# Performance work log

Hardware: AMD Instinct MI355X
Metric: run time of the kernel (lower is better)

## Reference

```python
import jax, jax.numpy as jnp
import numpy as np

B, S, D, H, I, E, K, L, C = 4, 1024, 512, 8, 2048, 8, 2, 4, 4
D2 = D // 2
EPS = 1e-5  # torch LayerNorm default


def _ln(x, w, b):
    m = jnp.mean(x, -1, keepdims=True)
    v = jnp.mean((x - m) ** 2, -1, keepdims=True)
    return (x - m) * jax.lax.rsqrt(v + EPS) * w + b


def setup_inputs() -> dict:
    key = jax.random.key(0)
    ks = iter(jax.random.split(key, 40))
    n = lambda shp, s=0.02: jax.random.normal(next(ks), shp, dtype=jnp.float32) * s
    return {
        'embeddings': jax.random.normal(next(ks), (B, S, D), jnp.float32),
        'attention_mask': jnp.ones((B, S), jnp.float32),
        'in_w': n((L, 3 * D, D)), 'in_b': jnp.zeros((L, 3 * D)),
        'out_w': n((L, D, D)), 'out_b': jnp.zeros((L, D)),
        'ln1_w': jnp.ones((L, D)), 'ln1_b': jnp.zeros((L, D)),
        'ln2_w': jnp.ones((L, D)), 'ln2_b': jnp.zeros((L, D)),
        'gate_w': n((L, E, D)),
        'e_w1': n((L, E, D, I)), 'e_b1': jnp.zeros((L, E, I)),
        'e_w2': n((L, E, I, D)), 'e_b2': jnp.zeros((L, E, D)),
        'mln_w': jnp.ones((L, D)), 'mln_b': jnp.zeros((L, D)),
        'fln_w': jnp.ones((D,)), 'fln_b': jnp.zeros((D,)),
        'pool_w': n((D, D)), 'pool_b': jnp.zeros((D,)),
        'cls_w': n((C, D)), 'cls_b': jnp.zeros((C,)),
        'cf_w1': n((D2, D)), 'cf_b1': jnp.zeros((D2,)),
        'cf_w2': n((1, D2)), 'cf_b2': jnp.zeros((1,)),
    }


def _forward(embeddings, attention_mask, in_w, in_b, out_w, out_b, ln1_w, ln1_b,
             ln2_w, ln2_b, gate_w, e_w1, e_b1, e_w2, e_b2, mln_w, mln_b,
             fln_w, fln_b, pool_w, pool_b, cls_w, cls_b, cf_w1, cf_b1, cf_w2, cf_b2):
    x = embeddings
    dh = D // H
    total_aux = jnp.float32(0.0)
    for l in range(L):
        # --- self-attention (eval mode, dropout off) ---
        h = _ln(x, ln1_w[l], ln1_b[l])
        qkv = h @ in_w[l].T + in_b[l]                       # (B,S,3D)
        q, k, v = jnp.split(qkv, 3, axis=-1)
        q = q.reshape(B, S, H, dh).transpose(0, 2, 1, 3)
        k = k.reshape(B, S, H, dh).transpose(0, 2, 1, 3)
        v = v.reshape(B, S, H, dh).transpose(0, 2, 1, 3)
        scores = jnp.einsum('bhqd,bhkd->bhqk', q, k) / (dh ** 0.5)
        attn = jax.nn.softmax(scores, axis=-1)
        ctx = jnp.einsum('bhqk,bhkd->bhqd', attn, v).transpose(0, 2, 1, 3).reshape(B, S, D)
        x = x + (ctx @ out_w[l].T + out_b[l])
        # --- MoE FFN (residual is the post-norm2 tensor, per source) ---
        h = _ln(x, ln2_w[l], ln2_b[l])
        flat = h.reshape(-1, D)                             # (T,D)
        probs = jax.nn.softmax(flat @ gate_w[l].T, axis=-1) # (T,E)
        vals, idx = jax.lax.top_k(probs, K)                 # (T,K)
        vals = vals / vals.sum(-1, keepdims=True)
        onehot = jax.nn.one_hot(idx, E, dtype=flat.dtype)   # (T,K,E)
        comb = jnp.einsum('tk,tke->te', vals, onehot)       # (T,E) per-expert weight, 0 if not selected
        mid = jax.nn.gelu(jnp.einsum('td,edf->tef', flat, e_w1[l]) + e_b1[l], approximate=False)
        eout = jnp.einsum('tef,efd->ted', mid, e_w2[l]) + e_b2[l]
        moe_out = jnp.einsum('ted,te->td', eout, comb).reshape(B, S, D)
        moe_out = moe_out * attention_mask[..., None]
        x = _ln(h + moe_out, mln_w[l], mln_b[l])
        usage = onehot.sum((0, 1)) / flat.shape[0]
        total_aux = total_aux + jnp.mean((usage - 1.0 / E) ** 2)
    # --- head ---
    x = _ln(x, fln_w, fln_b)
    me = attention_mask[..., None]
    pooled = (x * me).sum(1) / jnp.maximum(me.sum(1), 1e-9)
    pooled = jnp.tanh(pooled @ pool_w.T + pool_b)
    logits = pooled @ cls_w.T + cls_b
    conf = jax.nn.sigmoid(jax.nn.relu(pooled @ cf_w1.T + cf_b1) @ cf_w2.T + cf_b2)
    return logits, total_aux / L, conf


def reference(embeddings, attention_mask, in_w, in_b, out_w, out_b, ln1_w, ln1_b,
              ln2_w, ln2_b, gate_w, e_w1, e_b1, e_w2, e_b2, mln_w, mln_b,
              fln_w, fln_b, pool_w, pool_b, cls_w, cls_b, cf_w1, cf_b1, cf_w2, cf_b2):
    return _forward(embeddings, attention_mask, in_w, in_b, out_w, out_b, ln1_w, ln1_b,
                    ln2_w, ln2_b, gate_w, e_w1, e_b1, e_w2, e_b2, mln_w, mln_b,
                    fln_w, fln_b, pool_w, pool_b, cls_w, cls_b, cf_w1, cf_b1, cf_w2, cf_b2)
```

## Files before the change

kernel.cpp:

```cpp
#include <hip/hip_runtime.h>
#include <math.h>

#define B_ 4
#define S_ 1024
#define D_ 512
#define H_ 8
#define DH_ 64
#define I_ 2048
#define E_ 8
#define L_ 4
#define T_ 4096

using bf16x8 = __attribute__((ext_vector_type(8))) __bf16;
using f32x4  = __attribute__((ext_vector_type(4))) float;

typedef __attribute__((address_space(1))) const void gvoid;
typedef __attribute__((address_space(3))) void lvoid;
__device__ __forceinline__ void gl_lds16(const void* g, void* l){
  __builtin_amdgcn_global_load_lds((gvoid*)g, (lvoid*)l, 16, 0, 0);
}

__device__ __forceinline__ float wred_sum(float v){
#pragma unroll
  for(int m=32;m>0;m>>=1) v += __shfl_xor(v, m, 64);
  return v;
}
__device__ __forceinline__ unsigned short f2bf(float f){
  unsigned x = __float_as_uint(f);
  unsigned r = (x + 0x7FFFu + ((x>>16)&1u)) >> 16;
  return (unsigned short)r;
}
__device__ __forceinline__ float bf2f(unsigned short u){
  return __uint_as_float(((unsigned)u)<<16);
}
__device__ __forceinline__ unsigned pk2(float a, float b){
  return (unsigned)f2bf(a) | ((unsigned)f2bf(b)<<16);
}

template<int BM, int BN, bool MOE, bool GATHER, bool OUT_BF16, int ACT, bool ADD_IN, bool VT>
__global__ __launch_bounds__(512)
void gemm_k(const unsigned short* __restrict__ A, const unsigned short* __restrict__ Bv,
            void* Cp, const float* __restrict__ bias, const float* addin,
            int M, int N, int K, int lda, int ldb, int ldc,
            int hdiv, long sAb, long sAh, long sBb, long sBh, long sCb, long sCh,
            float scale,
            const int* __restrict__ moff, const int* __restrict__ mcnt,
            const int* __restrict__ rowtok, const int* __restrict__ btab,
            long sBe, int biasStride, int nby, unsigned short* __restrict__ vtp)
{
  constexpr int BK = 64;
  constexpr int WM = BM/2, WN = BN/4, FM = WM/16, FNN = WN/16;
  constexpr int RPC = 64;
  constexpr int SHPC = 4096;
  constexpr int NA = BM/RPC, NB = BN/RPC;
  __shared__ unsigned short As[2*BM*BK];
  __shared__ unsigned short Bs[2*BN*BK];

  const int tid = threadIdx.x, wid = tid>>6, lane = tid&63;
  const int wy = wid>>2, wx = wid&3, ln16 = lane&15;

  const int nwg = gridDim.x, cpx = nwg >> 3;
  const int lin = blockIdx.x;
  const int wg  = (lin & 7)*cpx + (lin >> 3);
  const int bxi = wg / nby, byi = wg % nby;

  int m0 = bxi*BM;
  const int n0 = byi*BN;

  float* Cf = nullptr; unsigned short* Ch = nullptr;
  const float* biasp = bias;
  const unsigned short* Bp = Bv;
  int seg = 0, cnt = M;

  if constexpr (MOE){
    int tv = btab[bxi];
    if (tv < 0) return;
    int e = tv>>8;
    m0 = (tv&255)*BM;
    seg = moff[e]; cnt = mcnt[e];
    Bp = Bv + (long)e*sBe;
    if constexpr (OUT_BF16) Ch = (unsigned short*)Cp; else Cf = (float*)Cp;
    if (biasp) biasp += (long)e*biasStride;
  } else {
    int z = blockIdx.z, zb = z/hdiv, zh = z%hdiv;
    A  += (long)zb*sAb + (long)zh*sAh;
    Bp += (long)zb*sBb + (long)zh*sBh;
    long coff = (long)zb*sCb + (long)zh*sCh;
    if constexpr (OUT_BF16) Ch = (unsigned short*)Cp + coff; else Cf = ((float*)Cp) + coff;
    if constexpr (ADD_IN) addin += coff;
  }

  const int srow = tid >> 3;
  const int scol = ((tid & 7) ^ (srow & 7)) * 8;
  long ga[NA], gb[NB];
#pragma unroll
  for (int j=0; j<NA; j++){
    int r = m0 + j*RPC + srow;
    if constexpr (MOE){
      r = min(r, cnt-1);
      long gr = GATHER ? (long)rowtok[seg+r] : (long)(seg+r);
      ga[j] = gr*lda + scol;
    } else {
      ga[j] = (long)min(r, M-1)*lda + scol;
    }
  }
#pragma unroll
  for (int j=0; j<NB; j++){
    int bn = min(n0 + j*RPC + srow, N-1);
    gb[j] = (long)bn*ldb + scol;
  }

  f32x4 acc[FM][FNN];
#pragma unroll
  for(int i=0;i<FM;i++)
#pragma unroll
    for(int j=0;j<FNN;j++){ f32x4 z = {0.f,0.f,0.f,0.f}; acc[i][j] = z; }

  const int nt = K/BK;
  const int rsw = ln16 & 7;
  const int u0 = ((lane>>4)     ^ rsw) * 8;
  const int u1 = ((4+(lane>>4)) ^ rsw) * 8;

#pragma unroll
  for (int j=0; j<NA; j++) gl_lds16(A + ga[j], As + j*SHPC + wid*512);
#pragma unroll
  for (int j=0; j<NB; j++) gl_lds16(Bp + gb[j], Bs + j*SHPC + wid*512);

  for (int t = 0; t < nt; ++t){
    const int cb = t & 1;
    const unsigned short* Ab = As + cb*BM*BK;
    const unsigned short* Bb = Bs + cb*BN*BK;
    unsigned short* An = As + (cb^1)*BM*BK;
    unsigned short* Bn = Bs + (cb^1)*BN*BK;
    const bool pf = (t+1 < nt);
    const long k0n = (long)(t+1)*BK;

    asm volatile("s_waitcnt vmcnt(0)" ::: "memory");
    __builtin_amdgcn_s_barrier();
    __builtin_amdgcn_sched_barrier(0);

    if (pf){
#pragma unroll
      for (int j=0; j<NA; j++) gl_lds16(A + ga[j] + k0n, An + j*SHPC + wid*512);
    }
    {
      bf16x8 fa[FM], fb[FNN];
#pragma unroll
      for(int i=0;i<FM;i++) fa[i] = *(const bf16x8*)&Ab[(wy*WM + i*16 + ln16)*BK + u0];
#pragma unroll
      for(int j=0;j<FNN;j++) fb[j] = *(const bf16x8*)&Bb[(wx*WN + j*16 + ln16)*BK + u0];
      __builtin_amdgcn_s_setprio(1);
#pragma unroll
      for(int i=0;i<FM;i++)
#pragma unroll
        for(int j=0;j<FNN;j++)
          acc[i][j] = __builtin_amdgcn_mfma_f32_16x16x32_bf16(fa[i], fb[j], acc[i][j], 0, 0, 0);
      __builtin_amdgcn_s_setprio(0);
    }
    if (pf){
#pragma unroll
      for (int j=0; j<NB; j++) gl_lds16(Bp + gb[j] + k0n, Bn + j*SHPC + wid*512);
    }
    {
      bf16x8 fa[FM], fb[FNN];
#pragma unroll
      for(int i=0;i<FM;i++) fa[i] = *(const bf16x8*)&Ab[(wy*WM + i*16 + ln16)*BK + u1];
#pragma unroll
      for(int j=0;j<FNN;j++) fb[j] = *(const bf16x8*)&Bb[(wx*WN + j*16 + ln16)*BK + u1];
      __builtin_amdgcn_s_setprio(1);
#pragma unroll
      for(int i=0;i<FM;i++)
#pragma unroll
        for(int j=0;j<FNN;j++)
          acc[i][j] = __builtin_amdgcn_mfma_f32_16x16x32_bf16(fa[i], fb[j], acc[i][j], 0, 0, 0);
      __builtin_amdgcn_s_setprio(0);
    }
  }

  if constexpr (VT){
    if (n0 >= 1024){
#pragma unroll
      for(int i=0;i<FM;i++){
        int mbase = m0 + wy*WM + i*16 + (lane>>4)*4;
        int bb = mbase >> 10;
        int k4 = mbase & 1023;
#pragma unroll
        for(int j=0;j<FNN;j++){
          int n = n0 + wx*WN + j*16 + ln16;
          float bv = biasp ? biasp[n] : 0.f;
          int hh = (n - 1024) >> 6, dd = (n - 1024) & 63;
          f32x4 v = acc[i][j];
          ushort4 pkv;
          pkv.x = f2bf(v[0]*scale + bv);
          pkv.y = f2bf(v[1]*scale + bv);
          pkv.z = f2bf(v[2]*scale + bv);
          pkv.w = f2bf(v[3]*scale + bv);
          *(ushort4*)(vtp + (long)(bb*8 + hh)*65536 + (long)dd*1024 + k4) = pkv;
        }
      }
      return;
    }
  }

#pragma unroll
  for(int i=0;i<FM;i++){
    int mbase = m0 + wy*WM + i*16 + (lane>>4)*4;
#pragma unroll
    for(int j=0;j<FNN;j++){
      int n = n0 + wx*WN + j*16 + ln16;
      float bv = biasp ? biasp[n] : 0.f;
      f32x4 v = acc[i][j];
#pragma unroll
      for(int r=0;r<4;r++){
        int m = mbase + r;
        if (m < cnt){
          float x = v[r]*scale + bv;
          if constexpr (ACT == 1) x = 0.5f*x*(1.f + erff(x*0.70710678118654752f));
          long ci = (long)(MOE ? seg + m : m)*ldc + n;
          if constexpr (ADD_IN) x += addin[ci];
          if constexpr (OUT_BF16) Ch[ci] = f2bf(x);
          else Cf[ci] = x;
        }
      }
    }
  }
}

__global__ __launch_bounds__(256)
void flash_k(const unsigned short* __restrict__ qkvb, const unsigned short* __restrict__ Vt,
             unsigned short* __restrict__ ctx)
{
  __shared__ unsigned short Pl[4][16*72];
  const int qt = blockIdx.x, z = blockIdx.y, b = z>>3, h = z&7;
  const int wid = threadIdx.x>>6, lane = threadIdx.x&63;
  const int ln16 = lane&15, g = lane>>4;
  const int q0 = qt*64 + wid*16;
  unsigned short* Pw = &Pl[wid][0];

  const unsigned short* Qp = qkvb + (long)(b*1024 + q0 + ln16)*1536 + h*64 + g*8;
  bf16x8 qf0 = *(const bf16x8*)Qp;
  bf16x8 qf1 = *(const bf16x8*)(Qp + 32);
  const unsigned short* Kbase = qkvb + (long)b*1024*1536 + 512 + h*64 + g*8;
  const unsigned short* Vbase = Vt + (long)z*65536 + g*8;

  float m_s[4], l_s[4];
  f32x4 oacc[4];
#pragma unroll
  for(int r=0;r<4;r++){ m_s[r] = -1e30f; l_s[r] = 0.f; }
#pragma unroll
  for(int j=0;j<4;j++){ f32x4 zz = {0.f,0.f,0.f,0.f}; oacc[j] = zz; }

  for (int t = 0; t < 16; ++t){
    bf16x8 kf[4][2], vf[4][2];
#pragma unroll
    for(int j=0;j<4;j++){
      const unsigned short* kp = Kbase + (long)(t*64 + j*16 + ln16)*1536;
      kf[j][0] = *(const bf16x8*)kp;
      kf[j][1] = *(const bf16x8*)(kp + 32);
      const unsigned short* vp = Vbase + (long)(j*16 + ln16)*1024 + t*64;
      vf[j][0] = *(const bf16x8*)vp;
      vf[j][1] = *(const bf16x8*)(vp + 32);
    }
    f32x4 sacc[4];
#pragma unroll
    for(int j=0;j<4;j++){ f32x4 zz = {0.f,0.f,0.f,0.f}; sacc[j] = zz; }
#pragma unroll
    for(int j=0;j<4;j++){
      sacc[j] = __builtin_amdgcn_mfma_f32_16x16x32_bf16(qf0, kf[j][0], sacc[j], 0,0,0);
      sacc[j] = __builtin_amdgcn_mfma_f32_16x16x32_bf16(qf1, kf[j][1], sacc[j], 0,0,0);
    }
#pragma unroll
    for(int j=0;j<4;j++)
#pragma unroll
      for(int r=0;r<4;r++) sacc[j][r] *= 0.125f;
    float alpha[4];
#pragma unroll
    for(int r=0;r<4;r++){
      float mx = fmaxf(fmaxf(sacc[0][r], sacc[1][r]), fmaxf(sacc[2][r], sacc[3][r]));
#pragma unroll
      for(int m=1;m<16;m<<=1) mx = fmaxf(mx, __shfl_xor(mx, m, 64));
      float mn = fmaxf(m_s[r], mx);
      alpha[r] = __expf(m_s[r] - mn);
      m_s[r] = mn;
    }
#pragma unroll
    for(int j=0;j<4;j++)
#pragma unroll
      for(int r=0;r<4;r++) sacc[j][r] = __expf(sacc[j][r] - m_s[r]);
#pragma unroll
    for(int r=0;r<4;r++){
      float rs = sacc[0][r]+sacc[1][r]+sacc[2][r]+sacc[3][r];
#pragma unroll
      for(int m=1;m<16;m<<=1) rs += __shfl_xor(rs, m, 64);
      l_s[r] = l_s[r]*alpha[r] + rs;
    }
#pragma unroll
    for(int j=0;j<4;j++)
#pragma unroll
      for(int r=0;r<4;r++) oacc[j][r] *= alpha[r];
#pragma unroll
    for(int j=0;j<4;j++)
#pragma unroll
      for(int r=0;r<4;r++)
        Pw[(g*4+r)*72 + j*16 + ln16] = f2bf(sacc[j][r]);
    bf16x8 pf0 = *(const bf16x8*)&Pw[ln16*72 + g*8];
    bf16x8 pf1 = *(const bf16x8*)&Pw[ln16*72 + 32 + g*8];
#pragma unroll
    for(int j=0;j<4;j++){
      oacc[j] = __builtin_amdgcn_mfma_f32_16x16x32_bf16(pf0, vf[j][0], oacc[j], 0,0,0);
      oacc[j] = __builtin_amdgcn_mfma_f32_16x16x32_bf16(pf1, vf[j][1], oacc[j], 0,0,0);
    }
  }
#pragma unroll
  for(int r=0;r<4;r++){
    float inv = 1.f/l_s[r];
    long row = (long)(b*1024 + q0 + g*4 + r)*512 + h*64;
#pragma unroll
    for(int j=0;j<4;j++)
      ctx[row + j*16 + ln16] = f2bf(oacc[j][r]*inv);
  }
}

template<bool OUT_BF16>
__global__ __launch_bounds__(256)
void ln_w_k(const float* __restrict__ in, const float* __restrict__ w,
            const float* __restrict__ bb, void* __restrict__ outp)
{
  int row = blockIdx.x*4 + (threadIdx.x>>6), lane = threadIdx.x&63;
  const float4* p = (const float4*)(in + (long)row*512 + lane*8);
  float4 a = p[0], c = p[1];
  float s = a.x+a.y+a.z+a.w + c.x+c.y+c.z+c.w;
  float q = a.x*a.x+a.y*a.y+a.z*a.z+a.w*a.w + c.x*c.x+c.y*c.y+c.z*c.z+c.w*c.w;
  s = wred_sum(s); q = wred_sum(q);
  float mean = s*(1.f/512.f);
  float var  = q*(1.f/512.f) - mean*mean;
  float inv  = rsqrtf(var + 1e-5f);
  const float4* wp = (const float4*)(w + lane*8);
  const float4* bp = (const float4*)(bb + lane*8);
  float4 w0 = wp[0], w1 = wp[1], b0 = bp[0], b1 = bp[1];
  float o0 = (a.x-mean)*inv*w0.x + b0.x, o1 = (a.y-mean)*inv*w0.y + b0.y;
  float o2 = (a.z-mean)*inv*w0.z + b0.z, o3 = (a.w-mean)*inv*w0.w + b0.w;
  float o4 = (c.x-mean)*inv*w1.x + b1.x, o5 = (c.y-mean)*inv*w1.y + b1.y;
  float o6 = (c.z-mean)*inv*w1.z + b1.z, o7 = (c.w-mean)*inv*w1.w + b1.w;
  if constexpr (OUT_BF16){
    *(uint4*)((unsigned short*)outp + (long)row*512 + lane*8) =
      make_uint4(pk2(o0,o1), pk2(o2,o3), pk2(o4,o5), pk2(o6,o7));
  } else {
    float4* op = (float4*)((float*)outp + (long)row*512 + lane*8);
    op[0] = make_float4(o0,o1,o2,o3);
    op[1] = make_float4(o4,o5,o6,o7);
  }
}

__global__ __launch_bounds__(256)
void ln2route_k(const float* __restrict__ in, const float* __restrict__ w,
                const float* __restrict__ bb, unsigned short* __restrict__ h2,
                const float* __restrict__ gw,
                int* __restrict__ tok_e, float* __restrict__ tok_w)
{
  int tok = blockIdx.x*4 + (threadIdx.x>>6), lane = threadIdx.x&63;
  const float4* p = (const float4*)(in + (long)tok*512 + lane*8);
  float4 a = p[0], c = p[1];
  float s = a.x+a.y+a.z+a.w + c.x+c.y+c.z+c.w;
  float q = a.x*a.x+a.y*a.y+a.z*a.z+a.w*a.w + c.x*c.x+c.y*c.y+c.z*c.z+c.w*c.w;
  s = wred_sum(s); q = wred_sum(q);
  float mean = s*(1.f/512.f);
  float var  = q*(1.f/512.f) - mean*mean;
  float inv  = rsqrtf(var + 1e-5f);
  const float4* wp = (const float4*)(w + lane*8);
  const float4* bp = (const float4*)(bb + lane*8);
  float4 w0 = wp[0], w1 = wp[1], b0 = bp[0], b1 = bp[1];
  float o[8];
  o[0] = (a.x-mean)*inv*w0.x + b0.x; o[1] = (a.y-mean)*inv*w0.y + b0.y;
  o[2] = (a.z-mean)*inv*w0.z + b0.z; o[3] = (a.w-mean)*inv*w0.w + b0.w;
  o[4] = (c.x-mean)*inv*w1.x + b1.x; o[5] = (c.y-mean)*inv*w1.y + b1.y;
  o[6] = (c.z-mean)*inv*w1.z + b1.z; o[7] = (c.w-mean)*inv*w1.w + b1.w;
  *(uint4*)(h2 + (long)tok*512 + lane*8) =
    make_uint4(pk2(o[0],o[1]), pk2(o[2],o[3]), pk2(o[4],o[5]), pk2(o[6],o[7]));
  float lg[8];
#pragma unroll
  for(int e=0;e<8;e++){
    const float4* gr = (const float4*)(gw + e*512 + lane*8);
    float4 g0 = gr[0], g1 = gr[1];
    float d = o[0]*g0.x + o[1]*g0.y + o[2]*g0.z + o[3]*g0.w
            + o[4]*g1.x + o[5]*g1.y + o[6]*g1.z + o[7]*g1.w;
    lg[e] = wred_sum(d);
  }
  if (lane == 0){
    float mx = lg[0];
#pragma unroll
    for(int e=1;e<8;e++) mx = fmaxf(mx, lg[e]);
    float pr[8];
#pragma unroll
    for(int e=0;e<8;e++) pr[e] = expf(lg[e]-mx);
    int e0 = 0; float p0 = pr[0];
#pragma unroll
    for(int e=1;e<8;e++) if (pr[e] > p0){ p0 = pr[e]; e0 = e; }
    int e1 = -1; float p1 = -1.f;
#pragma unroll
    for(int e=0;e<8;e++) if (e != e0 && pr[e] > p1){ p1 = pr[e]; e1 = e; }
    float invp = 1.f/(p0+p1);
    tok_e[2*tok] = e0; tok_e[2*tok+1] = e1;
    tok_w[2*tok] = p0*invp; tok_w[2*tok+1] = p1*invp;
  }
}

__global__ __launch_bounds__(1024)
void plan_scatter_k(const int* __restrict__ tok_e, const float* __restrict__ tok_w,
                    int* __restrict__ offs, int* __restrict__ cnts, float* __restrict__ aux,
                    int* __restrict__ btab, int* __restrict__ btab64,
                    int* __restrict__ rowtok, float* __restrict__ roww, int* __restrict__ rowof)
{
  __shared__ int hist[8];
  __shared__ int offsS[8];
  __shared__ int base[8];
  const int t = threadIdx.x;
  if (t < 8) hist[t] = 0;
  __syncthreads();
  int e[8]; float w[8];
#pragma unroll
  for (int i=0;i<8;i++){
    e[i] = tok_e[t + i*1024];
    w[i] = tok_w[t + i*1024];
    atomicAdd(&hist[e[i]], 1);
  }
  __syncthreads();
  if (t == 0){
    int o = 0, idx = 0, idx2 = 0; float a = 0.f;
    for (int ee=0; ee<8; ee++){
      offsS[ee] = o;
      int c = hist[ee];
      o += c;
      float u = (float)c*(1.f/4096.f) - 0.125f;
      a += u*u;
      int nb = (c + 127) >> 7;
      for (int j=0;j<nb;j++) btab[idx++] = (ee<<8)|j;
      int nb2 = (c + 63) >> 6;
      for (int j=0;j<nb2;j++) btab64[idx2++] = (ee<<8)|j;
    }
    while (idx < 80) btab[idx++] = -1;
    while (idx2 < 144) btab64[idx2++] = -1;
    *aux += a*(1.f/8.f);
  }
  __syncthreads();
  if (t < 8){
    cnts[t] = hist[t];
    offs[t] = offsS[t];
    base[t] = offsS[t];
  }
  __syncthreads();
#pragma unroll
  for (int i=0;i<8;i++){
    int pos = atomicAdd(&base[e[i]], 1);
    int gi = t + i*1024;
    rowtok[pos] = gi>>1;
    roww[pos] = w[i];
    rowof[gi] = pos;
  }
}

template<bool OUT2_BF16>
__global__ __launch_bounds__(256)
void ln_moe_k(const float* __restrict__ eout, const int* __restrict__ rowof,
              const float* __restrict__ roww, const float* __restrict__ mask,
              const unsigned short* __restrict__ h2,
              const float* __restrict__ w, const float* __restrict__ bb,
              float* __restrict__ outp,
              const float* __restrict__ w2, const float* __restrict__ b2,
              void* __restrict__ out2)
{
  int tok = blockIdx.x*4 + (threadIdx.x>>6), lane = threadIdx.x&63;
  int r0 = rowof[2*tok], r1 = rowof[2*tok+1];
  float w0w = roww[r0], w1w = roww[r1], mk = mask[tok];
  const float4* ap = (const float4*)(eout + (long)r0*512 + lane*8);
  const float4* bp2 = (const float4*)(eout + (long)r1*512 + lane*8);
  float4 a0 = ap[0], a1 = ap[1], c0 = bp2[0], c1 = bp2[1];
  uint4 hu = *(const uint4*)(h2 + (long)tok*512 + lane*8);
  const unsigned short* hh = (const unsigned short*)&hu;
  float v[8];
  v[0] = bf2f(hh[0]) + (a0.x*w0w + c0.x*w1w)*mk;
  v[1] = bf2f(hh[1]) + (a0.y*w0w + c0.y*w1w)*mk;
  v[2] = bf2f(hh[2]) + (a0.z*w0w + c0.z*w1w)*mk;
  v[3] = bf2f(hh[3]) + (a0.w*w0w + c0.w*w1w)*mk;
  v[4] = bf2f(hh[4]) + (a1.x*w0w + c1.x*w1w)*mk;
  v[5] = bf2f(hh[5]) + (a1.y*w0w + c1.y*w1w)*mk;
  v[6] = bf2f(hh[6]) + (a1.z*w0w + c1.z*w1w)*mk;
  v[7] = bf2f(hh[7]) + (a1.w*w0w + c1.w*w1w)*mk;
  float s = 0.f, q = 0.f;
#pragma unroll
  for(int i=0;i<8;i++){ s += v[i]; q += v[i]*v[i]; }
  s = wred_sum(s); q = wred_sum(q);
  float mean = s*(1.f/512.f);
  float var  = q*(1.f/512.f) - mean*mean;
  float inv  = rsqrtf(var + 1e-5f);
  const float4* wp = (const float4*)(w + lane*8);
  const float4* bpp = (const float4*)(bb + lane*8);
  float4 w0 = wp[0], w1 = wp[1], b0 = bpp[0], b1 = bpp[1];
  float wv[8] = {w0.x,w0.y,w0.z,w0.w,w1.x,w1.y,w1.z,w1.w};
  float bv[8] = {b0.x,b0.y,b0.z,b0.w,b1.x,b1.y,b1.z,b1.w};
  float o[8];
#pragma unroll
  for(int i=0;i<8;i++) o[i] = (v[i]-mean)*inv*wv[i]+bv[i];
  float4* op = (float4*)(outp + (long)tok*512 + lane*8);
  op[0] = make_float4(o[0], o[1], o[2], o[3]);
  op[1] = make_float4(o[4], o[5], o[6], o[7]);
  float s2 = 0.f, q2 = 0.f;
#pragma unroll
  for(int i=0;i<8;i++){ s2 += o[i]; q2 += o[i]*o[i]; }
  s2 = wred_sum(s2); q2 = wred_sum(q2);
  float mean2 = s2*(1.f/512.f);
  float var2  = q2*(1.f/512.f) - mean2*mean2;
  float inv2  = rsqrtf(var2 + 1e-5f);
  const float4* wp2 = (const float4*)(w2 + lane*8);
  const float4* bp3 = (const float4*)(b2 + lane*8);
  float4 x0 = wp2[0], x1 = wp2[1], y0 = bp3[0], y1 = bp3[1];
  float wv2[8] = {x0.x,x0.y,x0.z,x0.w,x1.x,x1.y,x1.z,x1.w};
  float bv2[8] = {y0.x,y0.y,y0.z,y0.w,y1.x,y1.y,y1.z,y1.w};
  float o2[8];
#pragma unroll
  for(int i=0;i<8;i++) o2[i] = (o[i]-mean2)*inv2*wv2[i]+bv2[i];
  if constexpr (OUT2_BF16){
    *(uint4*)((unsigned short*)out2 + (long)tok*512 + lane*8) =
      make_uint4(pk2(o2[0],o2[1]), pk2(o2[2],o2[3]), pk2(o2[4],o2[5]), pk2(o2[6],o2[7]));
  } else {
    float4* op2 = (float4*)((float*)out2 + (long)tok*512 + lane*8);
    op2[0] = make_float4(o2[0], o2[1], o2[2], o2[3]);
    op2[1] = make_float4(o2[4], o2[5], o2[6], o2[7]);
  }
}

__global__ __launch_bounds__(256)
void transpose_cast_k(const float* __restrict__ in, unsigned short* __restrict__ outp,
                      int R, int C, int ZL)
{
  __shared__ float tile[64][65];
  int t = threadIdx.x;
  int rr = t>>2, cc = (t&3)*16;
  int cc2 = t>>2, rr2 = (t&3)*16;
  int c0 = blockIdx.x*64, r0 = blockIdx.y*64;
  for (int zi = 0; zi < ZL; ++zi){
    long zoff = (long)(blockIdx.z*ZL + zi) * R * C;
    const float* pin = in + zoff + (long)(r0+rr)*C + c0 + cc;
    float4 v0=*(const float4*)pin, v1=*(const float4*)(pin+4), v2=*(const float4*)(pin+8), v3=*(const float4*)(pin+12);
    __syncthreads();
    tile[rr][cc+0]=v0.x; tile[rr][cc+1]=v0.y; tile[rr][cc+2]=v0.z; tile[rr][cc+3]=v0.w;
    tile[rr][cc+4]=v1.x; tile[rr][cc+5]=v1.y; tile[rr][cc+6]=v1.z; tile[rr][cc+7]=v1.w;
    tile[rr][cc+8]=v2.x; tile[rr][cc+9]=v2.y; tile[rr][cc+10]=v2.z; tile[rr][cc+11]=v2.w;
    tile[rr][cc+12]=v3.x; tile[rr][cc+13]=v3.y; tile[rr][cc+14]=v3.z; tile[rr][cc+15]=v3.w;
    __syncthreads();
    unsigned tmp[8];
#pragma unroll
    for(int jj=0;jj<8;jj++)
      tmp[jj] = pk2(tile[rr2+2*jj][cc2], tile[rr2+2*jj+1][cc2]);
    uint4* dst = (uint4*)(outp + zoff + (long)(c0+cc2)*R + r0 + rr2);
    dst[0] = make_uint4(tmp[0],tmp[1],tmp[2],tmp[3]);
    dst[1] = make_uint4(tmp[4],tmp[5],tmp[6],tmp[7]);
  }
}

__global__ __launch_bounds__(256)
void cast_bf16_k(const float* __restrict__ in, unsigned short* __restrict__ outp, int n8)
{
  for (int i = blockIdx.x*256 + threadIdx.x; i < n8; i += gridDim.x*256){
    const float4* p = (const float4*)(in + (long)i*8);
    float4 a = p[0], b = p[1];
    *(uint4*)(outp + (long)i*8) = make_uint4(pk2(a.x,a.y), pk2(a.z,a.w), pk2(b.x,b.y), pk2(b.z,b.w));
  }
}

__global__ __launch_bounds__(256)
void pool2_k(const float* __restrict__ h, const float* __restrict__ mask, float* __restrict__ pooled)
{
  int b = blockIdx.x, sc = blockIdx.y, t = threadIdx.x;
  float a0 = 0.f, a1 = 0.f;
  const float* mb = mask + b*1024 + sc*32;
  const float* hbase = h + ((long)b*1024 + sc*32)*512;
  for (int s = 0; s < 32; ++s){
    float mk = mb[s];
    const float* r = hbase + (long)s*512;
    a0 += r[t]*mk; a1 += r[t+256]*mk;
  }
  pooled[((b*32 + sc)*512) + t] = a0;
  pooled[((b*32 + sc)*512) + t + 256] = a1;
}

__global__ __launch_bounds__(256)
void head_final_k(const float* __restrict__ pooled, const float* __restrict__ mask,
                  const float* __restrict__ pool_w, const float* __restrict__ pool_b,
                  const float* __restrict__ cls_w, const float* __restrict__ cls_b,
                  const float* __restrict__ cf_w1, const float* __restrict__ cf_b1,
                  const float* __restrict__ cf_w2, const float* __restrict__ cf_b2,
                  const float* __restrict__ aux, float* __restrict__ out)
{
  int b = blockIdx.x, t = threadIdx.x, wid = t>>6, lane = t&63;
  __shared__ __align__(16) float pld[512];
  __shared__ __align__(16) float p2[512];
  __shared__ float red[4];
  float ds = 0.f;
  for(int s=t; s<1024; s+=256) ds += mask[b*1024 + s];
  ds = wred_sum(ds);
  if (lane==0) red[wid] = ds;
  __syncthreads();
  float denom = fmaxf(red[0]+red[1]+red[2]+red[3], 1e-9f);
  float s0 = 0.f, s1 = 0.f;
#pragma unroll
  for(int sc=0;sc<32;sc++){
    s0 += pooled[((b*32+sc)*512) + t];
    s1 += pooled[((b*32+sc)*512) + t + 256];
  }
  pld[t]     = s0/denom;
  pld[t+256] = s1/denom;
  __syncthreads();
#pragma unroll
  for(int jj=0;jj<2;jj++){
    int j = t + jj*256;
    const float4* wr = (const float4*)(pool_w + (long)j*512);
    float acc = 0.f;
    for(int i=0;i<128;i++){
      float4 w4 = wr[i]; float4 x4 = ((const float4*)pld)[i];
      acc += w4.x*x4.x + w4.y*x4.y + w4.z*x4.z + w4.w*x4.w;
    }
    p2[j] = tanhf(acc + pool_b[j]);
  }
  __syncthreads();
  if (t < 4){
    const float4* wr = (const float4*)(cls_w + (long)t*512);
    float acc = 0.f;
    for(int i=0;i<128;i++){
      float4 w4 = wr[i]; float4 x4 = ((const float4*)p2)[i];
      acc += w4.x*x4.x + w4.y*x4.y + w4.z*x4.z + w4.w*x4.w;
    }
    out[b*4 + t] = acc + cls_b[t];
  }
  {
    const float4* wr = (const float4*)(cf_w1 + (long)t*512);
    float acc = 0.f;
    for(int i=0;i<128;i++){
      float4 w4 = wr[i]; float4 x4 = ((const float4*)p2)[i];
      acc += w4.x*x4.x + w4.y*x4.y + w4.z*x4.z + w4.w*x4.w;
    }
    acc = fmaxf(acc + cf_b1[t], 0.f) * cf_w2[t];
    acc = wred_sum(acc);
    __syncthreads();
    if (lane==0) red[wid] = acc;
    __syncthreads();
    if (t == 0){
      float sum = red[0]+red[1]+red[2]+red[3];
      out[17 + b] = 1.f/(1.f + expf(-(sum + cf_b2[0])));
    }
  }
  if (b == 0 && t == 0) out[16] = aux[0]*0.25f;
}

extern "C" void kernel_launch(void* const* d_in, const int* in_sizes, int n_in,
                              void* d_out, int out_size, void* d_ws, size_t ws_size,
                              hipStream_t stream)
{
  (void)in_sizes; (void)n_in; (void)out_size;
  const float* emb    = (const float*)d_in[0];
  const float* mask   = (const float*)d_in[1];
  const float* in_w   = (const float*)d_in[2];
  const float* in_b   = (const float*)d_in[3];
  const float* out_w  = (const float*)d_in[4];
  const float* out_b  = (const float*)d_in[5];
  const float* ln1_w  = (const float*)d_in[6];
  const float* ln1_b  = (const float*)d_in[7];
  const float* ln2_w  = (const float*)d_in[8];
  const float* ln2_b  = (const float*)d_in[9];
  const float* gate_w = (const float*)d_in[10];
  const float* e_w1   = (const float*)d_in[11];
  const float* e_b1   = (const float*)d_in[12];
  const float* e_w2   = (const float*)d_in[13];
  const float* e_b2   = (const float*)d_in[14];
  const float* mln_w  = (const float*)d_in[15];
  const float* mln_b  = (const float*)d_in[16];
  const float* fln_w  = (const float*)d_in[17];
  const float* fln_b  = (const float*)d_in[18];
  const float* pool_w = (const float*)d_in[19];
  const float* pool_b = (const float*)d_in[20];
  const float* cls_w  = (const float*)d_in[21];
  const float* cls_b  = (const float*)d_in[22];
  const float* cf_w1  = (const float*)d_in[23];
  const float* cf_b1  = (const float*)d_in[24];
  const float* cf_w2  = (const float*)d_in[25];
  const float* cf_b2  = (const float*)d_in[26];
  float* out = (float*)d_out;
  char* ws = (char*)d_ws;

  const size_t MiB = 1024*1024;
  if (ws_size < 218*MiB) return;

  float*          x     = (float*)(ws + 0*MiB);
  unsigned short* hb    = (unsigned short*)(ws + 8*MiB);
  unsigned short* qkvb  = (unsigned short*)(ws + 12*MiB);
  unsigned short* ctx   = (unsigned short*)(ws + 24*MiB);
  unsigned short* Vt    = (unsigned short*)(ws + 28*MiB);
  unsigned short* mid   = (unsigned short*)(ws + 32*MiB);
  float*          eout  = (float*)(ws + 64*MiB);
  float*          fout  = (float*)(ws + 64*MiB);
  unsigned short* w1t   = (unsigned short*)(ws + 80*MiB);
  unsigned short* w2t   = (unsigned short*)(ws + 144*MiB);
  unsigned short* inwb  = (unsigned short*)(ws + 208*MiB);
  unsigned short* outwb = (unsigned short*)(ws + 214*MiB);
  char* misc = ws + 216*MiB;
  int*   counts  = (int*)(misc + 0);
  int*   offs    = (int*)(misc + 64);
  float* aux     = (float*)(misc + 128);
  int*   btab    = (int*)(misc + 256);
  int*   btab64  = (int*)(misc + 1024);
  int*   tok_e   = (int*)(misc + 81920);
  float* tok_w   = (float*)(misc + 114688);
  int*   rowtok  = (int*)(misc + 147456);
  float* roww    = (float*)(misc + 180224);
  int*   rowof   = (int*)(misc + 212992);
  float* pooled  = (float*)(misc + 262144);

  hipMemsetAsync(aux, 0, 4, stream);
  cast_bf16_k<<<512, 256, 0, stream>>>(in_w, inwb, L_*3*D_*D_/8);
  cast_bf16_k<<<256, 256, 0, stream>>>(out_w, outwb, L_*D_*D_/8);
  transpose_cast_k<<<dim3(I_/64, D_/64, 4), 256, 0, stream>>>(e_w1, w1t, D_, I_, 8);
  transpose_cast_k<<<dim3(D_/64, I_/64, 4), 256, 0, stream>>>(e_w2, w2t, I_, D_, 8);

  ln_w_k<true><<<T_/4, 256, 0, stream>>>(emb, ln1_w, ln1_b, hb);

  for (int l=0; l<L_; l++){
    const float* inbl  = in_b  + (size_t)l*3*D_;
    const float* outbl = out_b + (size_t)l*D_;
    const float* gwl   = gate_w + (size_t)l*E_*D_;
    const float* eb1l  = e_b1 + (size_t)l*E_*I_;
    const float* eb2l  = e_b2 + (size_t)l*E_*D_;
    const unsigned short* inwbl  = inwb + (size_t)l*3*D_*D_;
    const unsigned short* outwbl = outwb + (size_t)l*D_*D_;
    const unsigned short* w1tl = w1t + (size_t)l*E_*I_*D_;
    const unsigned short* w2tl = w2t + (size_t)l*E_*D_*I_;

    gemm_k<64,128,false,false,true,0,false,true><<<dim3(768,1,1), 512, 0, stream>>>(
      hb, inwbl, qkvb, inbl, nullptr, T_, 3*D_, D_, D_, D_, 3*D_,
      1, 0,0,0,0,0,0, 1.f, nullptr, nullptr, nullptr, nullptr, 0, 0, 12, Vt);
    flash_k<<<dim3(16,32), 256, 0, stream>>>(qkvb, Vt, ctx);
    gemm_k<64,64,false,false,false,0,true,false><<<dim3(512,1,1), 512, 0, stream>>>(
      ctx, outwbl, x, outbl, (l == 0 ? emb : x), T_, D_, D_, D_, D_, D_,
      1, 0,0,0,0,0,0, 1.f, nullptr, nullptr, nullptr, nullptr, 0, 0, 8, nullptr);
    ln2route_k<<<T_/4, 256, 0, stream>>>(x, ln2_w + (size_t)l*D_, ln2_b + (size_t)l*D_,
                                         hb, gwl, tok_e, tok_w);
    plan_scatter_k<<<1, 1024, 0, stream>>>(tok_e, tok_w, offs, counts, aux, btab, btab64,
                                           rowtok, roww, rowof);
    gemm_k<128,64,true,true,true,1,false,false><<<dim3(2272,1,1), 512, 0, stream>>>(
      hb, w1tl, mid, eb1l, nullptr, 2*T_, I_, D_, D_, D_, I_,
      1, 0,0,0,0,0,0, 1.f, offs, counts, rowtok, btab, (long)I_*D_, I_, 32, nullptr);
    gemm_k<64,128,true,false,false,0,false,false><<<dim3(544,1,1), 512, 0, stream>>>(
      mid, w2tl, eout, eb2l, nullptr, 2*T_, D_, I_, I_, I_, D_,
      1, 0,0,0,0,0,0, 1.f, offs, counts, nullptr, btab64, (long)D_*I_, D_, 4, nullptr);
    if (l < 3){
      ln_moe_k<true><<<T_/4, 256, 0, stream>>>(eout, rowof, roww, mask, hb,
                                               mln_w + (size_t)l*D_, mln_b + (size_t)l*D_, x,
                                               ln1_w + (size_t)(l+1)*D_, ln1_b + (size_t)(l+1)*D_,
                                               (void*)hb);
    } else {
      ln_moe_k<false><<<T_/4, 256, 0, stream>>>(eout, rowof, roww, mask, hb,
                                                mln_w + (size_t)l*D_, mln_b + (size_t)l*D_, x,
                                                fln_w, fln_b, (void*)fout);
    }
  }
  pool2_k<<<dim3(4,32), 256, 0, stream>>>(fout, mask, pooled);
  head_final_k<<<4, 256, 0, stream>>>(pooled, mask, pool_w, pool_b, cls_w, cls_b,
                                      cf_w1, cf_b1, cf_w2, cf_b2, aux, out);
}
```

Measured before the change: 1.257 ms.

## Double-buffer K/V loads in flash attention and remap blocks per XCD

The flash attention kernel now prefetches the next K/V tile into a second register buffer while computing on the current one, hiding global load latency. Blocks launch on a 1D grid and are remapped so that consecutive block IDs, which are dealt out round-robin across XCDs, group each (batch, head) onto one XCD for L2 reuse of K/V. MFMA sections are wrapped with s_setprio, and launch bounds request 2 blocks per CU. The doubled register buffers raise register pressure, which may hurt occupancy or cause spills.

```diff
diff --git a/kernel.cpp b/kernel.cpp
--- a/kernel.cpp
+++ b/kernel.cpp
@@ -226,12 +226,14 @@
   }
 }
 
-__global__ __launch_bounds__(256)
+__global__ __launch_bounds__(256, 2)
 void flash_k(const unsigned short* __restrict__ qkvb, const unsigned short* __restrict__ Vt,
              unsigned short* __restrict__ ctx)
 {
   __shared__ unsigned short Pl[4][16*72];
-  const int qt = blockIdx.x, z = blockIdx.y, b = z>>3, h = z&7;
+  const int lin = blockIdx.x;
+  const int wg  = (lin & 7)*64 + (lin >> 3);
+  const int qt = wg & 15, z = wg >> 4, b = z>>3, h = z&7;
   const int wid = threadIdx.x>>6, lane = threadIdx.x&63;
   const int ln16 = lane&15, g = lane>>4;
   const int q0 = qt*64 + wid*16;
@@ -250,25 +252,30 @@
 #pragma unroll
   for(int j=0;j<4;j++){ f32x4 zz = {0.f,0.f,0.f,0.f}; oacc[j] = zz; }
 
-  for (int t = 0; t < 16; ++t){
-    bf16x8 kf[4][2], vf[4][2];
-#pragma unroll
-    for(int j=0;j<4;j++){
-      const unsigned short* kp = Kbase + (long)(t*64 + j*16 + ln16)*1536;
-      kf[j][0] = *(const bf16x8*)kp;
-      kf[j][1] = *(const bf16x8*)(kp + 32);
-      const unsigned short* vp = Vbase + (long)(j*16 + ln16)*1024 + t*64;
-      vf[j][0] = *(const bf16x8*)vp;
-      vf[j][1] = *(const bf16x8*)(vp + 32);
-    }
+  bf16x8 ka[4][2], va[4][2], kb[4][2], vb[4][2];
+
+#define LOADKV(T, KD, VD) do { \
+  _Pragma("unroll") \
+  for(int j=0;j<4;j++){ \
+    const unsigned short* kp = Kbase + (long)((T)*64 + j*16 + ln16)*1536; \
+    KD[j][0] = *(const bf16x8*)kp; \
+    KD[j][1] = *(const bf16x8*)(kp + 32); \
+    const unsigned short* vp = Vbase + (long)(j*16 + ln16)*1024 + (T)*64; \
+    VD[j][0] = *(const bf16x8*)vp; \
+    VD[j][1] = *(const bf16x8*)(vp + 32); \
+  } } while(0)
+
+  auto compute = [&](bf16x8 (&kf)[4][2], bf16x8 (&vf)[4][2]){
     f32x4 sacc[4];
 #pragma unroll
     for(int j=0;j<4;j++){ f32x4 zz = {0.f,0.f,0.f,0.f}; sacc[j] = zz; }
+    __builtin_amdgcn_s_setprio(1);
 #pragma unroll
     for(int j=0;j<4;j++){
       sacc[j] = __builtin_amdgcn_mfma_f32_16x16x32_bf16(qf0, kf[j][0], sacc[j], 0,0,0);
       sacc[j] = __builtin_amdgcn_mfma_f32_16x16x32_bf16(qf1, kf[j][1], sacc[j], 0,0,0);
     }
+    __builtin_amdgcn_s_setprio(0);
 #pragma unroll
     for(int j=0;j<4;j++)
 #pragma unroll
@@ -305,12 +312,24 @@
         Pw[(g*4+r)*72 + j*16 + ln16] = f2bf(sacc[j][r]);
     bf16x8 pf0 = *(const bf16x8*)&Pw[ln16*72 + g*8];
     bf16x8 pf1 = *(const bf16x8*)&Pw[ln16*72 + 32 + g*8];
+    __builtin_amdgcn_s_setprio(1);
 #pragma unroll
     for(int j=0;j<4;j++){
       oacc[j] = __builtin_amdgcn_mfma_f32_16x16x32_bf16(pf0, vf[j][0], oacc[j], 0,0,0);
       oacc[j] = __builtin_amdgcn_mfma_f32_16x16x32_bf16(pf1, vf[j][1], oacc[j], 0,0,0);
     }
-  }
+    __builtin_amdgcn_s_setprio(0);
+  };
+
+  LOADKV(0, ka, va);
+  for (int tt = 0; tt < 8; ++tt){
+    LOADKV(2*tt+1, kb, vb);
+    compute(ka, va);
+    if (tt < 7) LOADKV(2*tt+2, ka, va);
+    compute(kb, vb);
+  }
+#undef LOADKV
+
 #pragma unroll
   for(int r=0;r<4;r++){
     float inv = 1.f/l_s[r];
@@ -737,7 +756,7 @@
     gemm_k<64,128,false,false,true,0,false,true><<<dim3(768,1,1), 512, 0, stream>>>(
       hb, inwbl, qkvb, inbl, nullptr, T_, 3*D_, D_, D_, D_, 3*D_,
       1, 0,0,0,0,0,0, 1.f, nullptr, nullptr, nullptr, nullptr, 0, 0, 12, Vt);
-    flash_k<<<dim3(16,32), 256, 0, stream>>>(qkvb, Vt, ctx);
+    flash_k<<<dim3(512,1,1), 256, 0, stream>>>(qkvb, Vt, ctx);
     gemm_k<64,64,false,false,false,0,true,false><<<dim3(512,1,1), 512, 0, stream>>>(
       ctx, outwbl, x, outbl, (l == 0 ? emb : x), T_, D_, D_, D_, D_, D_,
       1, 0,0,0,0,0,0, 1.f, nullptr, nullptr, nullptr, nullptr, 0, 0, 8, nullptr);
```

Measured after the change: 1.251 ms. Within noise of the previous version (-0.5%).
